# Optimization experiments

Hardware: AMD Instinct MI355X
Metric: run time of the kernel (lower is better)

The kernel has to match this reference:

```python
import jax, jax.numpy as jnp
import numpy as np

KERNEL_SIZE = 7
DILATION = 1
DYNAMIC_SIZE = 3


def setup_inputs() -> dict:
    key = jax.random.key(0)
    # [B, 2*(channels+1), H, W]; channels = 8 filterable + (8+2) param channels
    x = jax.random.normal(key, (2, 18, 1024, 1024), dtype=jnp.float32)
    return {"input": x}


def _bilateral(filterable, params, kernel_size, dilation):
    # filterable: [B, C, H, W]; params: [B, C+2, H, W] (already negated squares)
    B, C, H, W = filterable.shape
    r = kernel_size // 2
    pad = r * dilation
    fp = jnp.pad(filterable, ((0, 0), (0, 0), (pad, pad), (pad, pad)))
    mp = jnp.pad(jnp.ones((B, 1, H, W), filterable.dtype),
                 ((0, 0), (0, 0), (pad, pad), (pad, pad)))  # validity mask
    range_p = params[:, :C]      # per-channel range coefficients (<= 0)
    sx = params[:, C]            # spatial x coefficient (<= 0)
    sy = params[:, C + 1]        # spatial y coefficient (<= 0)
    acc = jnp.zeros_like(filterable)
    wsum = jnp.zeros((B, H, W), filterable.dtype)
    for i in range(kernel_size):        # fixed small window: loop is structural
        for j in range(kernel_size):
            oy, ox = i * dilation, j * dilation
            fn = jax.lax.dynamic_slice(fp, (0, 0, oy, ox), (B, C, H, W))
            m = jax.lax.dynamic_slice(mp, (0, 0, oy, ox), (B, 1, H, W))[:, 0]
            d2 = (fn - filterable) ** 2
            dy2 = float(((i - r) * dilation) ** 2)
            dx2 = float(((j - r) * dilation) ** 2)
            logw = jnp.einsum('bchw,bchw->bhw', range_p, d2) + sx * dx2 + sy * dy2
            w = jnp.exp(logw) * m   # out-of-bounds taps masked to 0
            acc = acc + w[:, None] * fn
            wsum = wsum + w
    # center tap has weight exp(0)=1, so wsum >= 1 (no div-by-zero)
    return acc / wsum[:, None]


def reference(input):
    C_in = input.shape[1]
    channels = C_in // 2 - 1
    filterable = input[:, :channels]
    params = input[:, channels:]
    params = -(params * params)
    filtered = _bilateral(filterable, params, KERNEL_SIZE, DILATION)
    return filtered[:, :DYNAMIC_SIZE]
```

## Files before the change

### kernel.cpp

```cpp
#include <hip/hip_runtime.h>

namespace {

constexpr int H = 1024;
constexpr int W = 1024;
constexpr int PLANE = H * W;
constexpr int CIN = 18;
constexpr int C = 8;
constexpr int TX = 16;
constexpr int TY = 16;
constexpr int SW = TX + 6;
constexpr int SH = TY + 6;
constexpr int NPOS = SW * SH;
constexpr float LOG2E = 1.44269504088896340736f;

typedef _Float16 half2_t __attribute__((ext_vector_type(2)));
typedef _Float16 half8_t __attribute__((ext_vector_type(8)));

__device__ __forceinline__ float dot2acc(half2_t a, half2_t b, float c) {
#if defined(__has_builtin)
#if __has_builtin(__builtin_amdgcn_fdot2)
    return __builtin_amdgcn_fdot2(a, b, c, false);
#else
    return fmaf((float)a[0], (float)b[0], fmaf((float)a[1], (float)b[1], c));
#endif
#else
    return fmaf((float)a[0], (float)b[0], fmaf((float)a[1], (float)b[1], c));
#endif
}

__device__ __forceinline__ float fast_exp2(float x) {
#if defined(__has_builtin)
#if __has_builtin(__builtin_amdgcn_exp2f)
    return __builtin_amdgcn_exp2f(x);
#else
    return exp2f(x);
#endif
#else
    return exp2f(x);
#endif
}

template<bool INTERIOR>
__device__ __forceinline__ void run_tile(const float* __restrict__ inb,
                                         float* __restrict__ outb,
                                         half8_t* __restrict__ tile,
                                         float* __restrict__ msk,
                                         int gy0, int gx0)
{
    const int tx = threadIdx.x, ty = threadIdx.y;
    const int tid = ty * TX + tx;

    const int gy = gy0 + ty, gx = gx0 + tx;
    const int pofs = gy * W + gx;

    half2_t rp01, rp23, rp45, rp67, rps;
    {
        const float* pp = inb + (size_t)C * PLANE + pofs;
        float r[C];
#pragma unroll
        for (int c = 0; c < C; ++c) {
            float p = pp[(size_t)c * PLANE];
            r[c] = -(p * p) * LOG2E;
        }
        float px_ = pp[(size_t)8 * PLANE];
        float py_ = pp[(size_t)9 * PLANE];
        rp01 = half2_t{(_Float16)r[0], (_Float16)r[1]};
        rp23 = half2_t{(_Float16)r[2], (_Float16)r[3]};
        rp45 = half2_t{(_Float16)r[4], (_Float16)r[5]};
        rp67 = half2_t{(_Float16)r[6], (_Float16)r[7]};
        rps  = half2_t{(_Float16)(-(px_ * px_) * LOG2E),
                       (_Float16)(-(py_ * py_) * LOG2E)};
    }

    for (int idx = tid; idx < NPOS; idx += TX * TY) {
        int y = idx / SW;
        int x = idx - y * SW;
        int sy_ = gy0 + y - 3;
        int sx_ = gx0 + x - 3;
        half8_t hv;
        if (INTERIOR || ((unsigned)sy_ < (unsigned)H && (unsigned)sx_ < (unsigned)W)) {
            const float* p = inb + sy_ * W + sx_;
#pragma unroll
            for (int c = 0; c < C; ++c) hv[c] = (_Float16)p[(size_t)c * PLANE];
            if (!INTERIOR) msk[idx] = 1.0f;
        } else {
#pragma unroll
            for (int c = 0; c < C; ++c) hv[c] = (_Float16)0.0f;
            msk[idx] = 0.0f;
        }
        tile[idx] = hv;
    }
    __syncthreads();

    const half8_t* lp = tile + ty * SW + tx;
    const half8_t fc = lp[3 * SW + 3];

    float acc0 = 0.f, acc1 = 0.f, acc2 = 0.f, ws = 0.f;
#pragma unroll
    for (int i = 0; i < 7; ++i) {
        const half8_t* row = lp + i * SW;
        const float* mrow = msk + (ty + i) * SW + tx;
#pragma unroll
        for (int j = 0; j < 7; ++j) {
            half8_t q = row[j];
            half8_t d = q - fc;
            half8_t dd = d * d;
            const half2_t cst = half2_t{(_Float16)(float)((j - 3) * (j - 3)),
                                        (_Float16)(float)((i - 3) * (i - 3))};
            float lw = dot2acc(cst, rps, 0.0f);
            lw = dot2acc(__builtin_shufflevector(dd, dd, 0, 1), rp01, lw);
            lw = dot2acc(__builtin_shufflevector(dd, dd, 2, 3), rp23, lw);
            lw = dot2acc(__builtin_shufflevector(dd, dd, 4, 5), rp45, lw);
            lw = dot2acc(__builtin_shufflevector(dd, dd, 6, 7), rp67, lw);
            float w = fast_exp2(lw);
            if (!INTERIOR) w *= mrow[j];
            ws += w;
            acc0 = fmaf(w, (float)q[0], acc0);
            acc1 = fmaf(w, (float)q[1], acc1);
            acc2 = fmaf(w, (float)q[2], acc2);
        }
    }
    const float inv = 1.0f / ws;
    outb[pofs]             = acc0 * inv;
    outb[PLANE + pofs]     = acc1 * inv;
    outb[2 * PLANE + pofs] = acc2 * inv;
}

__global__ __launch_bounds__(TX * TY, 4) void bilateral_kernel(const float* __restrict__ in,
                                                               float* __restrict__ out)
{
    __shared__ __align__(16) half8_t tile[NPOS];
    __shared__ float msk[NPOS];
    const int b = blockIdx.z;
    const int gx0 = blockIdx.x * TX;
    const int gy0 = blockIdx.y * TY;
    const float* inb = in + (size_t)b * CIN * PLANE;
    float* outb = out + (size_t)b * 3 * PLANE;

    const bool interior = (gx0 >= 3) && (gx0 + TX + 3 <= W) &&
                          (gy0 >= 3) && (gy0 + TY + 3 <= H);
    if (interior)
        run_tile<true>(inb, outb, tile, msk, gy0, gx0);
    else
        run_tile<false>(inb, outb, tile, msk, gy0, gx0);
}

}

extern "C" void kernel_launch(void* const* d_in, const int* in_sizes, int n_in,
                              void* d_out, int out_size, void* d_ws, size_t ws_size,
                              hipStream_t stream)
{
    const float* in = (const float*)d_in[0];
    float* out = (float*)d_out;
    dim3 grid(W / TX, H / TY, 2);
    dim3 block(TX, TY);
    hipLaunchKernelGGL(bilateral_kernel, grid, block, 0, stream, in, out);
}
```

Before: 253.6 us.

## Compute two vertically adjacent output pixels per thread to share LDS row loads

Each thread now produces two vertically adjacent outputs, and the tile grows to 16x32 outputs with a 38-row halo. Each row of seven LDS neighbors is loaded once and used for both pixels, which reduces LDS reads per output and shrinks the halo overhead per tile. The spatial term is now computed in fp32 with an fma instead of an fp16 dot. The cost is more registers, which could reduce occupancy under the launch bound of 4, plus a larger shared tile and half as many blocks.

Measured after the change: 735.5 us. 190% more time.

```diff
diff --git a/kernel.cpp b/kernel.cpp
--- a/kernel.cpp
+++ b/kernel.cpp
@@ -9,8 +9,9 @@
 constexpr int C = 8;
 constexpr int TX = 16;
 constexpr int TY = 16;
+constexpr int TILE_H = 32;
 constexpr int SW = TX + 6;
-constexpr int SH = TY + 6;
+constexpr int SH = TILE_H + 6;
 constexpr int NPOS = SW * SH;
 constexpr float LOG2E = 1.44269504088896340736f;
 
@@ -51,80 +52,162 @@
     const int tx = threadIdx.x, ty = threadIdx.y;
     const int tid = ty * TX + tx;
 
-    const int gy = gy0 + ty, gx = gx0 + tx;
-    const int pofs = gy * W + gx;
-
-    half2_t rp01, rp23, rp45, rp67, rps;
+    const int o0 = gy0 + 2 * ty;
+    const int gx = gx0 + tx;
+    const int pofs0 = o0 * W + gx;
+
+    half2_t rp01_0, rp23_0, rp45_0, rp67_0;
+    half2_t rp01_1, rp23_1, rp45_1, rp67_1;
+    float sxf0, syf0, sxf1, syf1;
     {
-        const float* pp = inb + (size_t)C * PLANE + pofs;
-        float r[C];
+        const float* pp = inb + (size_t)C * PLANE + pofs0;
+        float r0[C], r1[C];
 #pragma unroll
         for (int c = 0; c < C; ++c) {
-            float p = pp[(size_t)c * PLANE];
-            r[c] = -(p * p) * LOG2E;
+            float p0 = pp[(size_t)c * PLANE];
+            float p1 = pp[(size_t)c * PLANE + W];
+            r0[c] = -(p0 * p0) * LOG2E;
+            r1[c] = -(p1 * p1) * LOG2E;
         }
-        float px_ = pp[(size_t)8 * PLANE];
-        float py_ = pp[(size_t)9 * PLANE];
-        rp01 = half2_t{(_Float16)r[0], (_Float16)r[1]};
-        rp23 = half2_t{(_Float16)r[2], (_Float16)r[3]};
-        rp45 = half2_t{(_Float16)r[4], (_Float16)r[5]};
-        rp67 = half2_t{(_Float16)r[6], (_Float16)r[7]};
-        rps  = half2_t{(_Float16)(-(px_ * px_) * LOG2E),
-                       (_Float16)(-(py_ * py_) * LOG2E)};
-    }
-
-    for (int idx = tid; idx < NPOS; idx += TX * TY) {
-        int y = idx / SW;
-        int x = idx - y * SW;
-        int sy_ = gy0 + y - 3;
-        int sx_ = gx0 + x - 3;
-        half8_t hv;
-        if (INTERIOR || ((unsigned)sy_ < (unsigned)H && (unsigned)sx_ < (unsigned)W)) {
-            const float* p = inb + sy_ * W + sx_;
-#pragma unroll
-            for (int c = 0; c < C; ++c) hv[c] = (_Float16)p[(size_t)c * PLANE];
-            if (!INTERIOR) msk[idx] = 1.0f;
-        } else {
-#pragma unroll
-            for (int c = 0; c < C; ++c) hv[c] = (_Float16)0.0f;
-            msk[idx] = 0.0f;
+        float px0 = pp[(size_t)8 * PLANE];
+        float py0 = pp[(size_t)9 * PLANE];
+        float px1 = pp[(size_t)8 * PLANE + W];
+        float py1 = pp[(size_t)9 * PLANE + W];
+        rp01_0 = half2_t{(_Float16)r0[0], (_Float16)r0[1]};
+        rp23_0 = half2_t{(_Float16)r0[2], (_Float16)r0[3]};
+        rp45_0 = half2_t{(_Float16)r0[4], (_Float16)r0[5]};
+        rp67_0 = half2_t{(_Float16)r0[6], (_Float16)r0[7]};
+        rp01_1 = half2_t{(_Float16)r1[0], (_Float16)r1[1]};
+        rp23_1 = half2_t{(_Float16)r1[2], (_Float16)r1[3]};
+        rp45_1 = half2_t{(_Float16)r1[4], (_Float16)r1[5]};
+        rp67_1 = half2_t{(_Float16)r1[6], (_Float16)r1[7]};
+        sxf0 = -(px0 * px0) * LOG2E;  syf0 = -(py0 * py0) * LOG2E;
+        sxf1 = -(px1 * px1) * LOG2E;  syf1 = -(py1 * py1) * LOG2E;
+    }
+
+#pragma unroll
+    for (int it = 0; it < 4; ++it) {
+        int idx = tid + it * (TX * TY);
+        if (idx < NPOS) {
+            int y = idx / SW;
+            int x = idx - y * SW;
+            int sy_ = gy0 + y - 3;
+            int sx_ = gx0 + x - 3;
+            half8_t hv;
+            if (INTERIOR || ((unsigned)sy_ < (unsigned)H && (unsigned)sx_ < (unsigned)W)) {
+                const float* p = inb + sy_ * W + sx_;
+#pragma unroll
+                for (int c = 0; c < C; ++c) hv[c] = (_Float16)p[(size_t)c * PLANE];
+                if (!INTERIOR) msk[idx] = 1.0f;
+            } else {
+#pragma unroll
+                for (int c = 0; c < C; ++c) hv[c] = (_Float16)0.0f;
+                msk[idx] = 0.0f;
+            }
+            tile[idx] = hv;
         }
-        tile[idx] = hv;
     }
     __syncthreads();
 
-    const half8_t* lp = tile + ty * SW + tx;
-    const half8_t fc = lp[3 * SW + 3];
-
-    float acc0 = 0.f, acc1 = 0.f, acc2 = 0.f, ws = 0.f;
-#pragma unroll
-    for (int i = 0; i < 7; ++i) {
-        const half8_t* row = lp + i * SW;
-        const float* mrow = msk + (ty + i) * SW + tx;
-#pragma unroll
-        for (int j = 0; j < 7; ++j) {
-            half8_t q = row[j];
-            half8_t d = q - fc;
-            half8_t dd = d * d;
-            const half2_t cst = half2_t{(_Float16)(float)((j - 3) * (j - 3)),
-                                        (_Float16)(float)((i - 3) * (i - 3))};
-            float lw = dot2acc(cst, rps, 0.0f);
-            lw = dot2acc(__builtin_shufflevector(dd, dd, 0, 1), rp01, lw);
-            lw = dot2acc(__builtin_shufflevector(dd, dd, 2, 3), rp23, lw);
-            lw = dot2acc(__builtin_shufflevector(dd, dd, 4, 5), rp45, lw);
-            lw = dot2acc(__builtin_shufflevector(dd, dd, 6, 7), rp67, lw);
-            float w = fast_exp2(lw);
-            if (!INTERIOR) w *= mrow[j];
-            ws += w;
-            acc0 = fmaf(w, (float)q[0], acc0);
-            acc1 = fmaf(w, (float)q[1], acc1);
-            acc2 = fmaf(w, (float)q[2], acc2);
-        }
-    }
-    const float inv = 1.0f / ws;
-    outb[pofs]             = acc0 * inv;
-    outb[PLANE + pofs]     = acc1 * inv;
-    outb[2 * PLANE + pofs] = acc2 * inv;
+    const half8_t* lp = tile + (2 * ty) * SW + tx;
+    const half8_t fc0 = lp[3 * SW + 3];
+    const half8_t fc1 = lp[4 * SW + 3];
+
+    float a00 = 0.f, a01 = 0.f, a02 = 0.f, ws0 = 0.f;
+    float a10 = 0.f, a11 = 0.f, a12 = 0.f, ws1 = 0.f;
+
+    half8_t q0_, q1_, q2_, q3_, q4_, q5_, q6_;
+
+#define LOADROW(I) do { const half8_t* lq_ = lp + (I) * SW;              \
+        q0_ = lq_[0]; q1_ = lq_[1]; q2_ = lq_[2]; q3_ = lq_[3];          \
+        q4_ = lq_[4]; q5_ = lq_[5]; q6_ = lq_[6]; } while (0)
+
+#define PIXA(Q, J) do {                                                  \
+        half8_t d_ = (Q) - fc0;                                          \
+        half8_t dd_ = d_ * d_;                                           \
+        float lw_ = fmaf((float)(((J) - 3) * ((J) - 3)), sxf0, rs0_);    \
+        lw_ = dot2acc(__builtin_shufflevector(dd_, dd_, 0, 1), rp01_0, lw_); \
+        lw_ = dot2acc(__builtin_shufflevector(dd_, dd_, 2, 3), rp23_0, lw_); \
+        lw_ = dot2acc(__builtin_shufflevector(dd_, dd_, 4, 5), rp45_0, lw_); \
+        lw_ = dot2acc(__builtin_shufflevector(dd_, dd_, 6, 7), rp67_0, lw_); \
+        float w_ = fast_exp2(lw_);                                       \
+        if (!INTERIOR) w_ *= mrow_[(J)];                                 \
+        ws0 += w_;                                                       \
+        a00 = fmaf(w_, (float)(Q)[0], a00);                              \
+        a01 = fmaf(w_, (float)(Q)[1], a01);                              \
+        a02 = fmaf(w_, (float)(Q)[2], a02);                              \
+    } while (0)
+
+#define PIXB(Q, J) do {                                                  \
+        half8_t d_ = (Q) - fc1;                                          \
+        half8_t dd_ = d_ * d_;                                           \
+        float lw_ = fmaf((float)(((J) - 3) * ((J) - 3)), sxf1, rs1_);    \
+        lw_ = dot2acc(__builtin_shufflevector(dd_, dd_, 0, 1), rp01_1, lw_); \
+        lw_ = dot2acc(__builtin_shufflevector(dd_, dd_, 2, 3), rp23_1, lw_); \
+        lw_ = dot2acc(__builtin_shufflevector(dd_, dd_, 4, 5), rp45_1, lw_); \
+        lw_ = dot2acc(__builtin_shufflevector(dd_, dd_, 6, 7), rp67_1, lw_); \
+        float w_ = fast_exp2(lw_);                                       \
+        if (!INTERIOR) w_ *= mrow_[(J)];                                 \
+        ws1 += w_;                                                       \
+        a10 = fmaf(w_, (float)(Q)[0], a10);                              \
+        a11 = fmaf(w_, (float)(Q)[1], a11);                              \
+        a12 = fmaf(w_, (float)(Q)[2], a12);                              \
+    } while (0)
+
+#define ROW_COMMON(I)                                                    \
+        LOADROW(I);                                                      \
+        const float* mrow_ = msk + (2 * ty + (I)) * SW + tx;             \
+        (void)mrow_;
+
+#define ROW_FIRST(I) {                                                   \
+        ROW_COMMON(I)                                                    \
+        const float rs0_ = syf0 * (float)(((I) - 3) * ((I) - 3));        \
+        PIXA(q0_, 0); PIXA(q1_, 1); PIXA(q2_, 2); PIXA(q3_, 3);          \
+        PIXA(q4_, 4); PIXA(q5_, 5); PIXA(q6_, 6);                        \
+    }
+
+#define ROW_BOTH(I) {                                                    \
+        ROW_COMMON(I)                                                    \
+        const float rs0_ = syf0 * (float)(((I) - 3) * ((I) - 3));        \
+        const float rs1_ = syf1 * (float)(((I) - 4) * ((I) - 4));        \
+        PIXA(q0_, 0); PIXB(q0_, 0); PIXA(q1_, 1); PIXB(q1_, 1);          \
+        PIXA(q2_, 2); PIXB(q2_, 2); PIXA(q3_, 3); PIXB(q3_, 3);          \
+        PIXA(q4_, 4); PIXB(q4_, 4); PIXA(q5_, 5); PIXB(q5_, 5);          \
+        PIXA(q6_, 6); PIXB(q6_, 6);                                      \
+    }
+
+#define ROW_LAST(I) {                                                    \
+        ROW_COMMON(I)                                                    \
+        const float rs1_ = syf1 * (float)(((I) - 4) * ((I) - 4));        \
+        PIXB(q0_, 0); PIXB(q1_, 1); PIXB(q2_, 2); PIXB(q3_, 3);          \
+        PIXB(q4_, 4); PIXB(q5_, 5); PIXB(q6_, 6);                        \
+    }
+
+    ROW_FIRST(0)
+    ROW_BOTH(1)
+    ROW_BOTH(2)
+    ROW_BOTH(3)
+    ROW_BOTH(4)
+    ROW_BOTH(5)
+    ROW_BOTH(6)
+    ROW_LAST(7)
+
+#undef ROW_LAST
+#undef ROW_BOTH
+#undef ROW_FIRST
+#undef ROW_COMMON
+#undef PIXB
+#undef PIXA
+#undef LOADROW
+
+    const float inv0 = 1.0f / ws0;
+    const float inv1 = 1.0f / ws1;
+    outb[pofs0]                 = a00 * inv0;
+    outb[PLANE + pofs0]         = a01 * inv0;
+    outb[2 * PLANE + pofs0]     = a02 * inv0;
+    outb[pofs0 + W]             = a10 * inv1;
+    outb[PLANE + pofs0 + W]     = a11 * inv1;
+    outb[2 * PLANE + pofs0 + W] = a12 * inv1;
 }
 
 __global__ __launch_bounds__(TX * TY, 4) void bilateral_kernel(const float* __restrict__ in,
@@ -134,12 +217,12 @@
     __shared__ float msk[NPOS];
     const int b = blockIdx.z;
     const int gx0 = blockIdx.x * TX;
-    const int gy0 = blockIdx.y * TY;
+    const int gy0 = blockIdx.y * TILE_H;
     const float* inb = in + (size_t)b * CIN * PLANE;
     float* outb = out + (size_t)b * 3 * PLANE;
 
     const bool interior = (gx0 >= 3) && (gx0 + TX + 3 <= W) &&
-                          (gy0 >= 3) && (gy0 + TY + 3 <= H);
+                          (gy0 >= 3) && (gy0 + TILE_H + 3 <= H);
     if (interior)
         run_tile<true>(inb, outb, tile, msk, gy0, gx0);
     else
@@ -154,7 +237,7 @@
 {
     const float* in = (const float*)d_in[0];
     float* out = (float*)d_out;
-    dim3 grid(W / TX, H / TY, 2);
+    dim3 grid(W / TX, H / TILE_H, 2);
     dim3 block(TX, TY);
     hipLaunchKernelGGL(bilateral_kernel, grid, block, 0, stream, in, out);
 }
```
